# Performance work log

Measured on AMD Instinct MI355X. Metric: run time of the kernel, lower is better.

## Reference

```python
import jax, jax.numpy as jnp
import numpy as np

N = 50000   # nodes
E = 800000  # edges (before self-loops)
IN, HID, OUT = 128, 128, 64


def gcn_norm(edge_index, num_nodes):
    # add self loops with weight 1, then symmetric deg^-1/2 normalization
    loop = jnp.arange(num_nodes, dtype=edge_index.dtype)
    row = jnp.concatenate([edge_index[0], loop])
    col = jnp.concatenate([edge_index[1], loop])
    ew = jnp.ones(row.shape[0], dtype=jnp.float32)
    deg = jax.ops.segment_sum(ew, col, num_segments=num_nodes)
    dis = jnp.where(deg > 0, jax.lax.rsqrt(deg), 0.0)
    norm = dis[row] * ew * dis[col]
    return row, col, norm


def gcn_conv(x, row, col, norm, W, b):
    h = x @ W                                   # [N, F_out] dense GEMM
    msg = h[row] * norm[:, None]                # gather + scale over edges
    out = jax.ops.segment_sum(msg, col, num_segments=x.shape[0])  # scatter-add
    return out + b


def setup_inputs() -> dict:
    key = jax.random.key(0)
    k0, k1, k2, k3, k4, k5 = jax.random.split(key, 6)
    x = jax.random.normal(k0, (N, IN), dtype=jnp.float32)
    edge_index = jax.random.randint(k1, (2, E), 0, N, dtype=jnp.int32)
    # glorot-style init for linear weights, zeros for bias (PyG default)
    W1 = jax.random.normal(k2, (IN, HID), dtype=jnp.float32) * np.float32(np.sqrt(1.0 / IN))
    b1 = jnp.zeros((HID,), dtype=jnp.float32)
    W2 = jax.random.normal(k3, (HID, OUT), dtype=jnp.float32) * np.float32(np.sqrt(1.0 / HID))
    b2 = jnp.zeros((OUT,), dtype=jnp.float32)
    return {"x": x, "edge_index": edge_index, "W1": W1, "b1": b1, "W2": W2, "b2": b2}


def reference(x, edge_index, W1, b1, W2, b2):
    row, col, norm = gcn_norm(edge_index, x.shape[0])
    h = jax.nn.relu(gcn_conv(x, row, col, norm, W1, b1))
    # dropout is a no-op in eval mode (training=False)
    out = gcn_conv(h, row, col, norm, W2, b2)
    return out
```

## Files before the change

kernel.cpp:

```cpp
#include <hip/hip_runtime.h>
#include <hip/hip_fp16.h>


#define Nn 50000
#define Ne 800000
#define SCAN_B ((Nn + 1023) / 1024)

using f16x8 = _Float16 __attribute__((ext_vector_type(8)));
using f32x4 = float __attribute__((ext_vector_type(4)));

__global__ __launch_bounds__(256) void k_count(const int* __restrict__ col,
                                               int* __restrict__ degi,
                                               unsigned short* __restrict__ rank) {
  int e = blockIdx.x * 256 + threadIdx.x;
  if (e < Ne) rank[e] = (unsigned short)atomicAdd(&degi[col[e]], 1);
}

__global__ __launch_bounds__(1024) void k_scan1(const int* __restrict__ degi,
                                                int* __restrict__ rowptr,
                                                float* __restrict__ dis,
                                                int* __restrict__ bsum) {
  __shared__ int wsum[16];
  int tid = threadIdx.x;
  int lane = tid & 63, wid = tid >> 6;
  int i = blockIdx.x * 1024 + tid;
  int v = (i < Nn) ? degi[i] : 0;
  if (i < Nn) dis[i] = rsqrtf((float)(v + 1));
  int incl = v;
  #pragma unroll
  for (int off = 1; off < 64; off <<= 1) {
    int t = __shfl_up(incl, off);
    if (lane >= off) incl += t;
  }
  if (lane == 63) wsum[wid] = incl;
  __syncthreads();
  if (wid == 0) {
    int wv = (lane < 16) ? wsum[lane] : 0;
    #pragma unroll
    for (int off = 1; off < 16; off <<= 1) {
      int t = __shfl_up(wv, off);
      if (lane >= off) wv += t;
    }
    if (lane < 16) wsum[lane] = wv;
  }
  __syncthreads();
  int woff = (wid > 0) ? wsum[wid - 1] : 0;
  if (i < Nn) rowptr[i] = woff + incl - v;
  if (tid == 0) bsum[blockIdx.x] = wsum[15];
}

__global__ __launch_bounds__(1024) void k_scan3(int* __restrict__ rowptr,
                                                const int* __restrict__ bsum) {
  __shared__ int off_s;
  int tid = threadIdx.x;
  if (tid < 64) {
    int v = (tid < SCAN_B) ? bsum[tid] : 0;
    int incl = v;
    #pragma unroll
    for (int off = 1; off < 64; off <<= 1) {
      int t = __shfl_up(incl, off);
      if (tid >= off) incl += t;
    }
    if (tid == (int)blockIdx.x) off_s = incl - v;
    if (blockIdx.x == 0 && tid == SCAN_B - 1) rowptr[Nn] = incl;
  }
  __syncthreads();
  int i = blockIdx.x * 1024 + tid;
  if (i < Nn) rowptr[i] += off_s;
}

__global__ __launch_bounds__(256) void k_fill(const int* __restrict__ row,
                                              const int* __restrict__ col,
                                              const int* __restrict__ rowptr,
                                              const unsigned short* __restrict__ rank,
                                              unsigned short* __restrict__ csr) {
  int e = blockIdx.x * 256 + threadIdx.x;
  if (e >= Ne) return;
  int r = row[e], c = col[e];
  csr[rowptr[c] + (int)rank[e]] = (unsigned short)r;
}

template <int LDO>
__global__ __launch_bounds__(256) void k_gemm_mfma(const float* __restrict__ X,
                                                   const float* __restrict__ W,
                                                   __half* __restrict__ H, int n) {
  __shared__ _Float16 Xs[64 * 136];
  __shared__ _Float16 Wts[LDO * 136];
  const int tid = threadIdx.x;
  const int base = blockIdx.x * 64;

  {
    constexpr int C4 = LDO / 4;
    for (int idx4 = tid; idx4 < 32 * LDO; idx4 += 256) {
      int k = idx4 / C4;
      int c = (idx4 % C4) * 4;
      float4 wv = ((const float4*)W)[idx4];
      Wts[(c + 0) * 136 + k] = (_Float16)wv.x;
      Wts[(c + 1) * 136 + k] = (_Float16)wv.y;
      Wts[(c + 2) * 136 + k] = (_Float16)wv.z;
      Wts[(c + 3) * 136 + k] = (_Float16)wv.w;
    }
  }
  {
    for (int u = tid; u < 64 * 16; u += 256) {
      int r = u >> 4, seg = u & 15;
      int node = base + r;
      if (node >= n) node = n - 1;
      const float4* xg = (const float4*)(X + (size_t)node * 128 + seg * 8);
      float4 x0 = xg[0], x1 = xg[1];
      f16x8 hv;
      hv[0] = (_Float16)x0.x; hv[1] = (_Float16)x0.y;
      hv[2] = (_Float16)x0.z; hv[3] = (_Float16)x0.w;
      hv[4] = (_Float16)x1.x; hv[5] = (_Float16)x1.y;
      hv[6] = (_Float16)x1.z; hv[7] = (_Float16)x1.w;
      *(f16x8*)&Xs[r * 136 + seg * 8] = hv;
    }
  }
  __syncthreads();

  const int w = tid >> 6, lane = tid & 63;
  const int quad = lane >> 4, mrow = lane & 15;
  constexpr int NCT = LDO / 16;

  f32x4 acc[NCT];
  #pragma unroll
  for (int ct = 0; ct < NCT; ++ct) acc[ct] = (f32x4){0.f, 0.f, 0.f, 0.f};

  #pragma unroll
  for (int ko = 0; ko < 4; ++ko) {
    f16x8 av = *(const f16x8*)&Xs[(w * 16 + mrow) * 136 + ko * 32 + quad * 8];
    #pragma unroll
    for (int ct = 0; ct < NCT; ++ct) {
      f16x8 bv = *(const f16x8*)&Wts[(ct * 16 + mrow) * 136 + ko * 32 + quad * 8];
      acc[ct] = __builtin_amdgcn_mfma_f32_16x16x32_f16(av, bv, acc[ct], 0, 0, 0);
    }
  }

  #pragma unroll
  for (int ct = 0; ct < NCT; ++ct) {
    #pragma unroll
    for (int r = 0; r < 4; ++r) {
      int node = base + w * 16 + quad * 4 + r;
      if (node < n)
        H[(size_t)node * LDO + ct * 16 + mrow] = __float2half(acc[ct][r]);
    }
  }
}

__device__ __forceinline__ float2 h2f(unsigned int u) {
  return __half22float2(*(const __half2*)&u);
}

__global__ __launch_bounds__(256) void k_agg128(const __half* __restrict__ H,
                                                const unsigned short* __restrict__ csr,
                                                const int* __restrict__ rowptr,
                                                const float* __restrict__ dis,
                                                const float* __restrict__ bias,
                                                float* __restrict__ Out, int n) {
  const int wid = threadIdx.x >> 6, lane = threadIdx.x & 63;
  const int sub = lane >> 4, fl = lane & 15;
  int v = blockIdx.x * 16 + wid * 4 + sub;
  if (v >= n) return;
  int s = rowptr[v], e = rowptr[v + 1];
  float d = dis[v];
  float sw = d * d;
  const uint4* Hq = (const uint4*)H;
  uint4 hv = Hq[(size_t)v * 16 + fl];
  float2 p0 = h2f(hv.x), p1 = h2f(hv.y), p2 = h2f(hv.z), p3 = h2f(hv.w);
  float a0 = p0.x * sw, a1 = p0.y * sw, a2 = p1.x * sw, a3 = p1.y * sw;
  float a4 = p2.x * sw, a5 = p2.y * sw, a6 = p3.x * sw, a7 = p3.y * sw;
  constexpr int D = 6;
  int i = s;
  for (; i + D <= e; i += D) {
    int srcs[D];
    uint4 q[D];
    float wd[D];
    #pragma unroll
    for (int j = 0; j < D; ++j) srcs[j] = csr[i + j];
    #pragma unroll
    for (int j = 0; j < D; ++j) q[j] = Hq[(size_t)srcs[j] * 16 + fl];
    #pragma unroll
    for (int j = 0; j < D; ++j) wd[j] = dis[srcs[j]];
    #pragma unroll
    for (int j = 0; j < D; ++j) {
      float w = wd[j] * d;
      float2 t;
      t = h2f(q[j].x); a0 = fmaf(w, t.x, a0); a1 = fmaf(w, t.y, a1);
      t = h2f(q[j].y); a2 = fmaf(w, t.x, a2); a3 = fmaf(w, t.y, a3);
      t = h2f(q[j].z); a4 = fmaf(w, t.x, a4); a5 = fmaf(w, t.y, a5);
      t = h2f(q[j].w); a6 = fmaf(w, t.x, a6); a7 = fmaf(w, t.y, a7);
    }
  }
  if (i < e) {
    int srcs[D];
    uint4 q[D];
    float wd[D];
    #pragma unroll
    for (int j = 0; j < D; ++j) {
      int idx = (i + j < e) ? i + j : e - 1;
      srcs[j] = csr[idx];
    }
    #pragma unroll
    for (int j = 0; j < D; ++j) q[j] = Hq[(size_t)srcs[j] * 16 + fl];
    #pragma unroll
    for (int j = 0; j < D; ++j) wd[j] = dis[srcs[j]];
    #pragma unroll
    for (int j = 0; j < D; ++j) {
      float w = (i + j < e) ? wd[j] * d : 0.f;
      float2 t;
      t = h2f(q[j].x); a0 = fmaf(w, t.x, a0); a1 = fmaf(w, t.y, a1);
      t = h2f(q[j].y); a2 = fmaf(w, t.x, a2); a3 = fmaf(w, t.y, a3);
      t = h2f(q[j].z); a4 = fmaf(w, t.x, a4); a5 = fmaf(w, t.y, a5);
      t = h2f(q[j].w); a6 = fmaf(w, t.x, a6); a7 = fmaf(w, t.y, a7);
    }
  }
  const float4* Bq = (const float4*)bias;
  float4 b0 = Bq[fl * 2], b1 = Bq[fl * 2 + 1];
  float4 o0 = make_float4(fmaxf(a0 + b0.x, 0.f), fmaxf(a1 + b0.y, 0.f),
                          fmaxf(a2 + b0.z, 0.f), fmaxf(a3 + b0.w, 0.f));
  float4 o1 = make_float4(fmaxf(a4 + b1.x, 0.f), fmaxf(a5 + b1.y, 0.f),
                          fmaxf(a6 + b1.z, 0.f), fmaxf(a7 + b1.w, 0.f));
  float4* Oq = (float4*)(Out + (size_t)v * 128);
  Oq[fl * 2] = o0;
  Oq[fl * 2 + 1] = o1;
}

__global__ __launch_bounds__(256) void k_agg64(const __half* __restrict__ H,
                                               const unsigned short* __restrict__ csr,
                                               const int* __restrict__ rowptr,
                                               const float* __restrict__ dis,
                                               const float* __restrict__ bias,
                                               float* __restrict__ Out, int n) {
  const int wid = threadIdx.x >> 6, lane = threadIdx.x & 63;
  const int sub = lane >> 4, fl = lane & 15;
  int v = blockIdx.x * 16 + wid * 4 + sub;
  if (v >= n) return;
  int s = rowptr[v], e = rowptr[v + 1];
  float d = dis[v];
  float sw = d * d;
  const uint2* Hq = (const uint2*)H;
  uint2 hv = Hq[(size_t)v * 16 + fl];
  float2 p0 = h2f(hv.x), p1 = h2f(hv.y);
  float a0 = p0.x * sw, a1 = p0.y * sw, a2 = p1.x * sw, a3 = p1.y * sw;
  constexpr int D = 8;
  int i = s;
  for (; i + D <= e; i += D) {
    int srcs[D];
    uint2 q[D];
    float wd[D];
    #pragma unroll
    for (int j = 0; j < D; ++j) srcs[j] = csr[i + j];
    #pragma unroll
    for (int j = 0; j < D; ++j) q[j] = Hq[(size_t)srcs[j] * 16 + fl];
    #pragma unroll
    for (int j = 0; j < D; ++j) wd[j] = dis[srcs[j]];
    #pragma unroll
    for (int j = 0; j < D; ++j) {
      float w = wd[j] * d;
      float2 t;
      t = h2f(q[j].x); a0 = fmaf(w, t.x, a0); a1 = fmaf(w, t.y, a1);
      t = h2f(q[j].y); a2 = fmaf(w, t.x, a2); a3 = fmaf(w, t.y, a3);
    }
  }
  if (i < e) {
    int srcs[D];
    uint2 q[D];
    float wd[D];
    #pragma unroll
    for (int j = 0; j < D; ++j) {
      int idx = (i + j < e) ? i + j : e - 1;
      srcs[j] = csr[idx];
    }
    #pragma unroll
    for (int j = 0; j < D; ++j) q[j] = Hq[(size_t)srcs[j] * 16 + fl];
    #pragma unroll
    for (int j = 0; j < D; ++j) wd[j] = dis[srcs[j]];
    #pragma unroll
    for (int j = 0; j < D; ++j) {
      float w = (i + j < e) ? wd[j] * d : 0.f;
      float2 t;
      t = h2f(q[j].x); a0 = fmaf(w, t.x, a0); a1 = fmaf(w, t.y, a1);
      t = h2f(q[j].y); a2 = fmaf(w, t.x, a2); a3 = fmaf(w, t.y, a3);
    }
  }
  const float4* Bq = (const float4*)bias;
  float4 b = Bq[fl];
  float4 o = make_float4(a0 + b.x, a1 + b.y, a2 + b.z, a3 + b.w);
  ((float4*)(Out + (size_t)v * 64))[fl] = o;
}

extern "C" void kernel_launch(void* const* d_in, const int* in_sizes, int n_in,
                              void* d_out, int out_size, void* d_ws, size_t ws_size,
                              hipStream_t stream) {
  const float* x  = (const float*)d_in[0];
  const int*   ei = (const int*)d_in[1];
  const int*   row = ei;
  const int*   col = ei + Ne;
  const float* W1 = (const float*)d_in[2];
  const float* b1 = (const float*)d_in[3];
  const float* W2 = (const float*)d_in[4];
  const float* b2 = (const float*)d_in[5];
  float* out = (float*)d_out;

  char* ws = (char*)d_ws;
  size_t off = 0;
  auto alloc = [&](size_t bytes) -> void* {
    void* p = ws + off;
    off += (bytes + 255) & ~(size_t)255;
    return p;
  };
  int*    degi   = (int*)   alloc(Nn * sizeof(int));
  int*    rowptr = (int*)   alloc((Nn + 1) * sizeof(int));
  float*  dis    = (float*) alloc(Nn * sizeof(float));
  int*    bsum   = (int*)   alloc(64 * sizeof(int));
  unsigned short* rank = (unsigned short*)alloc((size_t)Ne * sizeof(unsigned short));
  unsigned short* csr  = (unsigned short*)alloc((size_t)Ne * sizeof(unsigned short));
  __half* H1     = (__half*)alloc((size_t)Nn * 128 * sizeof(__half));
  float*  H1b    = (float*) alloc((size_t)Nn * 128 * sizeof(float));
  __half* H2     = (__half*)alloc((size_t)Nn * 64 * sizeof(__half));

  hipMemsetAsync(degi, 0, Nn * sizeof(int), stream);

  const int EB  = (Ne + 255) / 256;
  const int NGB = (Nn + 15) / 16;
  const int GT  = (Nn + 63) / 64;

  k_count<<<EB, 256, 0, stream>>>(col, degi, rank);
  k_scan1<<<SCAN_B, 1024, 0, stream>>>(degi, rowptr, dis, bsum);
  k_scan3<<<SCAN_B, 1024, 0, stream>>>(rowptr, bsum);
  k_fill<<<EB, 256, 0, stream>>>(row, col, rowptr, rank, csr);

  k_gemm_mfma<128><<<GT, 256, 0, stream>>>(x, W1, H1, Nn);
  k_agg128<<<NGB, 256, 0, stream>>>(H1, csr, rowptr, dis, b1, H1b, Nn);

  k_gemm_mfma<64><<<GT, 256, 0, stream>>>(H1b, W2, H2, Nn);
  k_agg64<<<NGB, 256, 0, stream>>>(H2, csr, rowptr, dis, b2, out, Nn);
}
```

Measured before the change: 211.3 us.

## Fuse layer-1 aggregation with layer-2 GEMM via LDS and MFMA

The first-layer aggregation kernel now applies bias and ReLU, converts its 16 aggregated rows per block to fp16 in shared memory, and immediately multiplies them by W2 with MFMA. That writes the 64-wide fp16 H2 directly. This removes the fp32 H1b intermediate (a 25.6 MB write and reread) and one kernel launch. In exchange, every block reloads and transposes W2 into LDS, and the hidden activations are rounded to fp16 before the second GEMM.

```diff
diff --git a/kernel.cpp b/kernel.cpp
--- a/kernel.cpp
+++ b/kernel.cpp
@@ -151,78 +151,117 @@
   return __half22float2(*(const __half2*)&u);
 }
 
-__global__ __launch_bounds__(256) void k_agg128(const __half* __restrict__ H,
-                                                const unsigned short* __restrict__ csr,
-                                                const int* __restrict__ rowptr,
-                                                const float* __restrict__ dis,
-                                                const float* __restrict__ bias,
-                                                float* __restrict__ Out, int n) {
-  const int wid = threadIdx.x >> 6, lane = threadIdx.x & 63;
+__global__ __launch_bounds__(256) void k_agg128_gemm64(
+    const __half* __restrict__ H, const unsigned short* __restrict__ csr,
+    const int* __restrict__ rowptr, const float* __restrict__ dis,
+    const float* __restrict__ bias, const float* __restrict__ W2,
+    __half* __restrict__ H2, int n) {
+  __shared__ _Float16 Wts[64 * 136];
+  __shared__ _Float16 Hs[16 * 136];
+
+  const int tid = threadIdx.x;
+  const int wid = tid >> 6, lane = tid & 63;
   const int sub = lane >> 4, fl = lane & 15;
-  int v = blockIdx.x * 16 + wid * 4 + sub;
-  if (v >= n) return;
-  int s = rowptr[v], e = rowptr[v + 1];
-  float d = dis[v];
-  float sw = d * d;
-  const uint4* Hq = (const uint4*)H;
-  uint4 hv = Hq[(size_t)v * 16 + fl];
-  float2 p0 = h2f(hv.x), p1 = h2f(hv.y), p2 = h2f(hv.z), p3 = h2f(hv.w);
-  float a0 = p0.x * sw, a1 = p0.y * sw, a2 = p1.x * sw, a3 = p1.y * sw;
-  float a4 = p2.x * sw, a5 = p2.y * sw, a6 = p3.x * sw, a7 = p3.y * sw;
-  constexpr int D = 6;
-  int i = s;
-  for (; i + D <= e; i += D) {
-    int srcs[D];
-    uint4 q[D];
-    float wd[D];
-    #pragma unroll
-    for (int j = 0; j < D; ++j) srcs[j] = csr[i + j];
-    #pragma unroll
-    for (int j = 0; j < D; ++j) q[j] = Hq[(size_t)srcs[j] * 16 + fl];
-    #pragma unroll
-    for (int j = 0; j < D; ++j) wd[j] = dis[srcs[j]];
-    #pragma unroll
-    for (int j = 0; j < D; ++j) {
-      float w = wd[j] * d;
-      float2 t;
-      t = h2f(q[j].x); a0 = fmaf(w, t.x, a0); a1 = fmaf(w, t.y, a1);
-      t = h2f(q[j].y); a2 = fmaf(w, t.x, a2); a3 = fmaf(w, t.y, a3);
-      t = h2f(q[j].z); a4 = fmaf(w, t.x, a4); a5 = fmaf(w, t.y, a5);
-      t = h2f(q[j].w); a6 = fmaf(w, t.x, a6); a7 = fmaf(w, t.y, a7);
-    }
-  }
-  if (i < e) {
-    int srcs[D];
-    uint4 q[D];
-    float wd[D];
-    #pragma unroll
-    for (int j = 0; j < D; ++j) {
-      int idx = (i + j < e) ? i + j : e - 1;
-      srcs[j] = csr[idx];
-    }
-    #pragma unroll
-    for (int j = 0; j < D; ++j) q[j] = Hq[(size_t)srcs[j] * 16 + fl];
-    #pragma unroll
-    for (int j = 0; j < D; ++j) wd[j] = dis[srcs[j]];
-    #pragma unroll
-    for (int j = 0; j < D; ++j) {
-      float w = (i + j < e) ? wd[j] * d : 0.f;
-      float2 t;
-      t = h2f(q[j].x); a0 = fmaf(w, t.x, a0); a1 = fmaf(w, t.y, a1);
-      t = h2f(q[j].y); a2 = fmaf(w, t.x, a2); a3 = fmaf(w, t.y, a3);
-      t = h2f(q[j].z); a4 = fmaf(w, t.x, a4); a5 = fmaf(w, t.y, a5);
-      t = h2f(q[j].w); a6 = fmaf(w, t.x, a6); a7 = fmaf(w, t.y, a7);
-    }
-  }
-  const float4* Bq = (const float4*)bias;
-  float4 b0 = Bq[fl * 2], b1 = Bq[fl * 2 + 1];
-  float4 o0 = make_float4(fmaxf(a0 + b0.x, 0.f), fmaxf(a1 + b0.y, 0.f),
-                          fmaxf(a2 + b0.z, 0.f), fmaxf(a3 + b0.w, 0.f));
-  float4 o1 = make_float4(fmaxf(a4 + b1.x, 0.f), fmaxf(a5 + b1.y, 0.f),
-                          fmaxf(a6 + b1.z, 0.f), fmaxf(a7 + b1.w, 0.f));
-  float4* Oq = (float4*)(Out + (size_t)v * 128);
-  Oq[fl * 2] = o0;
-  Oq[fl * 2 + 1] = o1;
+  const int nb = wid * 4 + sub;
+  const int v = blockIdx.x * 16 + nb;
+
+  for (int idx4 = tid; idx4 < 2048; idx4 += 256) {
+    int k = idx4 >> 4;
+    int c = (idx4 & 15) * 4;
+    float4 wv = ((const float4*)W2)[idx4];
+    Wts[(c + 0) * 136 + k] = (_Float16)wv.x;
+    Wts[(c + 1) * 136 + k] = (_Float16)wv.y;
+    Wts[(c + 2) * 136 + k] = (_Float16)wv.z;
+    Wts[(c + 3) * 136 + k] = (_Float16)wv.w;
+  }
+
+  float a0 = 0, a1 = 0, a2 = 0, a3 = 0, a4 = 0, a5 = 0, a6 = 0, a7 = 0;
+  float d = 0.f;
+  if (v < n) {
+    int s = rowptr[v], e = rowptr[v + 1];
+    d = dis[v];
+    float sw = d * d;
+    const uint4* Hq = (const uint4*)H;
+    uint4 hv = Hq[(size_t)v * 16 + fl];
+    float2 p0 = h2f(hv.x), p1 = h2f(hv.y), p2 = h2f(hv.z), p3 = h2f(hv.w);
+    a0 = p0.x * sw; a1 = p0.y * sw; a2 = p1.x * sw; a3 = p1.y * sw;
+    a4 = p2.x * sw; a5 = p2.y * sw; a6 = p3.x * sw; a7 = p3.y * sw;
+    constexpr int D = 6;
+    int i = s;
+    for (; i + D <= e; i += D) {
+      int srcs[D];
+      uint4 q[D];
+      float wd[D];
+      #pragma unroll
+      for (int j = 0; j < D; ++j) srcs[j] = csr[i + j];
+      #pragma unroll
+      for (int j = 0; j < D; ++j) q[j] = Hq[(size_t)srcs[j] * 16 + fl];
+      #pragma unroll
+      for (int j = 0; j < D; ++j) wd[j] = dis[srcs[j]];
+      #pragma unroll
+      for (int j = 0; j < D; ++j) {
+        float w = wd[j] * d;
+        float2 t;
+        t = h2f(q[j].x); a0 = fmaf(w, t.x, a0); a1 = fmaf(w, t.y, a1);
+        t = h2f(q[j].y); a2 = fmaf(w, t.x, a2); a3 = fmaf(w, t.y, a3);
+        t = h2f(q[j].z); a4 = fmaf(w, t.x, a4); a5 = fmaf(w, t.y, a5);
+        t = h2f(q[j].w); a6 = fmaf(w, t.x, a6); a7 = fmaf(w, t.y, a7);
+      }
+    }
+    if (i < e) {
+      int srcs[D];
+      uint4 q[D];
+      float wd[D];
+      #pragma unroll
+      for (int j = 0; j < D; ++j) {
+        int idx = (i + j < e) ? i + j : e - 1;
+        srcs[j] = csr[idx];
+      }
+      #pragma unroll
+      for (int j = 0; j < D; ++j) q[j] = Hq[(size_t)srcs[j] * 16 + fl];
+      #pragma unroll
+      for (int j = 0; j < D; ++j) wd[j] = dis[srcs[j]];
+      #pragma unroll
+      for (int j = 0; j < D; ++j) {
+        float w = (i + j < e) ? wd[j] * d : 0.f;
+        float2 t;
+        t = h2f(q[j].x); a0 = fmaf(w, t.x, a0); a1 = fmaf(w, t.y, a1);
+        t = h2f(q[j].y); a2 = fmaf(w, t.x, a2); a3 = fmaf(w, t.y, a3);
+        t = h2f(q[j].z); a4 = fmaf(w, t.x, a4); a5 = fmaf(w, t.y, a5);
+        t = h2f(q[j].w); a6 = fmaf(w, t.x, a6); a7 = fmaf(w, t.y, a7);
+      }
+    }
+  }
+  {
+    const float4* Bq = (const float4*)bias;
+    float4 b0 = Bq[fl * 2], b1v = Bq[fl * 2 + 1];
+    f16x8 hrow;
+    hrow[0] = (_Float16)fmaxf(a0 + b0.x, 0.f);
+    hrow[1] = (_Float16)fmaxf(a1 + b0.y, 0.f);
+    hrow[2] = (_Float16)fmaxf(a2 + b0.z, 0.f);
+    hrow[3] = (_Float16)fmaxf(a3 + b0.w, 0.f);
+    hrow[4] = (_Float16)fmaxf(a4 + b1v.x, 0.f);
+    hrow[5] = (_Float16)fmaxf(a5 + b1v.y, 0.f);
+    hrow[6] = (_Float16)fmaxf(a6 + b1v.z, 0.f);
+    hrow[7] = (_Float16)fmaxf(a7 + b1v.w, 0.f);
+    *(f16x8*)&Hs[nb * 136 + fl * 8] = hrow;
+  }
+  __syncthreads();
+
+  const int quad = lane >> 4, mrow = lane & 15;
+  f32x4 acc = (f32x4){0.f, 0.f, 0.f, 0.f};
+  #pragma unroll
+  for (int ko = 0; ko < 4; ++ko) {
+    f16x8 av = *(const f16x8*)&Hs[mrow * 136 + ko * 32 + quad * 8];
+    f16x8 bv = *(const f16x8*)&Wts[(wid * 16 + mrow) * 136 + ko * 32 + quad * 8];
+    acc = __builtin_amdgcn_mfma_f32_16x16x32_f16(av, bv, acc, 0, 0, 0);
+  }
+  #pragma unroll
+  for (int r = 0; r < 4; ++r) {
+    int node = blockIdx.x * 16 + quad * 4 + r;
+    if (node < n)
+      H2[(size_t)node * 64 + wid * 16 + mrow] = __float2half(acc[r]);
+  }
 }
 
 __global__ __launch_bounds__(256) void k_agg64(const __half* __restrict__ H,
@@ -316,7 +355,6 @@
   unsigned short* rank = (unsigned short*)alloc((size_t)Ne * sizeof(unsigned short));
   unsigned short* csr  = (unsigned short*)alloc((size_t)Ne * sizeof(unsigned short));
   __half* H1     = (__half*)alloc((size_t)Nn * 128 * sizeof(__half));
-  float*  H1b    = (float*) alloc((size_t)Nn * 128 * sizeof(float));
   __half* H2     = (__half*)alloc((size_t)Nn * 64 * sizeof(__half));
 
   hipMemsetAsync(degi, 0, Nn * sizeof(int), stream);
@@ -331,8 +369,6 @@
   k_fill<<<EB, 256, 0, stream>>>(row, col, rowptr, rank, csr);
 
   k_gemm_mfma<128><<<GT, 256, 0, stream>>>(x, W1, H1, Nn);
-  k_agg128<<<NGB, 256, 0, stream>>>(H1, csr, rowptr, dis, b1, H1b, Nn);
-
-  k_gemm_mfma<64><<<GT, 256, 0, stream>>>(H1b, W2, H2, Nn);
+  k_agg128_gemm64<<<NGB, 256, 0, stream>>>(H1, csr, rowptr, dis, b1, W2, H2, Nn);
   k_agg64<<<NGB, 256, 0, stream>>>(H2, csr, rowptr, dis, b2, out, Nn);
 }
```

Result: no change. 207.5 us (-1.8%).
